# Kernel tuning notes

Measured on AMD Instinct MI355X. Metric: run time of the kernel, lower is better.

## Reference

```python
import jax, jax.numpy as jnp
import numpy as np

SIGMA = 1.0
EPSILON = 1.0
MAX_ITER = 10


def pairwise_kernel(x, y, sigma=SIGMA):
    # k = -||x-y||^2 / (2 sigma^2), shape [B, L, K]
    outer = jnp.einsum('bld,bkd->blk', x, y)
    nx = jnp.sum(x * x, axis=2)
    ny = jnp.sum(y * y, axis=2)
    dist = jnp.clip(nx[:, :, None] + ny[:, None, :] - 2.0 * outer, 0.0, None)
    return -dist / (2.0 * sigma ** 2)


def c_transform(potential, log_weight, kernel, epsilon=EPSILON):
    # rho=None => scale=1, lse = -eps * logsumexp(kernel/eps + (pot/eps + log_w))
    s = potential / epsilon + log_weight            # [B, K]
    operand = kernel / epsilon + s[:, None, :]      # [B, L, K]
    return -epsilon * jax.scipy.special.logsumexp(operand, axis=2)


def potentials(kxy, log_a, log_b):
    kyx = jnp.swapaxes(kxy, 1, 2)
    f0 = jnp.zeros_like(log_a)
    g0 = jnp.zeros_like(log_b)

    def step(carry, _):
        f, g = carry
        fn = c_transform(g, log_b, kxy)
        gn = c_transform(f, log_a, kyx)
        return ((fn + f) * 0.5, (gn + g) * 0.5), None

    (f, g), _ = jax.lax.scan(step, (f0, g0), None, length=MAX_ITER)
    return f, g


def sym_potential(x, log_a):
    kxx = pairwise_kernel(x, x)
    f0 = jnp.zeros_like(log_a)

    def step(f, _):
        fn = c_transform(f, log_a, kxx)
        return (fn + f) * 0.5, None

    f, _ = jax.lax.scan(step, f0, None, length=MAX_ITER)
    return f


def evaluate_potential(x, a, y, b, g):
    # phi_transform is identity for rho=None; scaled_dot_prod forward = sum(a*f, dim=1)
    kxy = pairwise_kernel(x, y)
    f = c_transform(g, jnp.log(b), kxy)
    return jnp.sum(a * f, axis=1)


def setup_inputs() -> dict:
    key = jax.random.key(0)
    k1, k2, k3, k4 = jax.random.split(key, 4)
    B, L, K, D = 8, 2048, 2048, 32
    x = jax.random.normal(k1, (B, L, D), dtype=jnp.float32)
    y = jax.random.normal(k2, (B, K, D), dtype=jnp.float32)
    a = jax.random.uniform(k3, (B, L), dtype=jnp.float32, minval=0.1, maxval=1.0)
    b = jax.random.uniform(k4, (B, K), dtype=jnp.float32, minval=0.1, maxval=1.0)
    a = a / jnp.sum(a, axis=1, keepdims=True)
    b = b / jnp.sum(b, axis=1, keepdims=True)
    return {"x": x, "a": a, "y": y, "b": b}


def reference(x, a, y, b):
    log_a, log_b = jnp.log(a), jnp.log(b)
    kxy = pairwise_kernel(x, y)
    f, g = potentials(kxy, log_a, log_b)
    dist = evaluate_potential(x, a, y, b, g) + evaluate_potential(y, b, x, a, f)
    fx = sym_potential(x, log_a)
    fy = sym_potential(y, log_b)
    ent_x = evaluate_potential(x, a, x, a, fx)
    ent_y = evaluate_potential(y, b, y, b, fy)
    return jnp.mean(dist - ent_x - ent_y)
```

## Files before the change

### kernel.cpp

```cpp
#include <hip/hip_runtime.h>
#include <math.h>

#define BATCH 8
#define NPT   2048
#define DIM   32
#define RPB   64
#define STRIPS (RPB / 16)
#define NBLKR (NPT / RPB)
#define CPW   (NPT / 4)
#define NT    (CPW / 16)
#define L2E   1.44269504088896f
#define BN    (BATCH * NPT)

typedef __attribute__((ext_vector_type(8))) _Float16 half8;
typedef __attribute__((ext_vector_type(4))) float floatx4;
typedef unsigned short u16;
typedef unsigned int u32;

__device__ __forceinline__ u16 f2h_bits(float v) {
    _Float16 h = (_Float16)v;
    return *(u16*)&h;
}
__device__ __forceinline__ float exp2v(float x) { return __builtin_amdgcn_exp2f(x); }

struct CtSet {
    const u16* Ah;
    const u16* Bh;
    const float* tls;
    const float* qX;
    const float* bmIn;
    const float* cwNext;
    const float* prev;
    float* out;
    float* tlsOut;
    float* bmOut;
};
struct CtArgs { CtSet s[4]; int average; };

__global__ __launch_bounds__(256, 4) void ct_kernel(CtArgs args) {
    const int bid  = blockIdx.x;
    const int batch = bid & 7;
    const int rest  = bid >> 3;
    const int slice = rest & 3;
    const int xb    = rest >> 2;
    const CtSet cs = args.s[slice];
    const int row0 = xb * RPB;
    const int tid  = threadIdx.x;
    const int w = tid >> 6, lane = tid & 63, n = lane & 15, quad = lane >> 4;
    const int qk = quad * 8;
    const size_t pbase = (size_t)batch * NPT * DIM;
    const size_t vbase = (size_t)batch * NPT;

    __shared__ float lsum[RPB][4];

    const u16* __restrict__ Ah = cs.Ah + pbase;
    const u16* __restrict__ Bh = cs.Bh + pbase;
    const float* __restrict__ tls = cs.tls + vbase;

    half8 ah[STRIPS];
    #pragma unroll
    for (int s = 0; s < STRIPS; s++) {
        size_t off = (size_t)(row0 + s * 16 + n) * DIM + qk;
        ah[s] = *(const half8*)(Ah + off);
    }

    float tmv = fmaxf(cs.bmIn[batch * 128 + lane], cs.bmIn[batch * 128 + 64 + lane]);
    #pragma unroll
    for (int m = 1; m < 64; m <<= 1) tmv = fmaxf(tmv, __shfl_xor(tmv, m, 64));
    const float Tmax = tmv;
    const float l2eTmax = L2E * Tmax;

    float sum[STRIPS][4];
    #pragma unroll
    for (int s = 0; s < STRIPS; s++)
        #pragma unroll
        for (int r = 0; r < 4; r++) sum[s][r] = 0.0f;

    const int c0 = w * CPW + n;
    const u16* bp = Bh + (size_t)c0 * DIM + qk;
    const float* tp = tls + c0;

    half8 bb[4];
    float tt[4];
    bb[0] = *(const half8*)bp;                       tt[0] = tp[0];
    bb[1] = *(const half8*)(bp + (size_t)16 * DIM);  tt[1] = tp[16];

    auto tile = [&](half8 b, float t) {
        float bias = t - l2eTmax;
        floatx4 ci = (floatx4){bias, bias, bias, bias};
        floatx4 acc[STRIPS];
        #pragma unroll
        for (int s = 0; s < STRIPS; s++)
            acc[s] = __builtin_amdgcn_mfma_f32_16x16x32_f16(ah[s], b, ci, 0, 0, 0);
        #pragma unroll
        for (int s = 0; s < STRIPS; s++)
            #pragma unroll
            for (int r = 0; r < 4; r++)
                sum[s][r] += exp2v(acc[s][r]);
    };

    #pragma unroll 1
    for (int ch = 0; ch < NT; ch += 4) {
        #pragma unroll
        for (int j = 0; j < 4; j++) {
            int nx = ch + j + 2;
            int nxc = nx < NT ? nx : NT - 1;
            bb[(j + 2) & 3] = *(const half8*)(bp + (size_t)nxc * 16 * DIM);
            tt[(j + 2) & 3] = tp[nxc * 16];
            tile(bb[j], tt[j]);
        }
    }

    #pragma unroll
    for (int s = 0; s < STRIPS; s++)
        #pragma unroll
        for (int r = 0; r < 4; r++) {
            float v = sum[s][r];
            #pragma unroll
            for (int m = 1; m < 16; m <<= 1) v += __shfl_xor(v, m, 64);
            if (n == 0) lsum[s * 16 + quad * 4 + r][w] = v;
        }
    __syncthreads();

    if (tid < RPB) {
        float T = (lsum[tid][0] + lsum[tid][1]) + (lsum[tid][2] + lsum[tid][3]);
        int l = row0 + tid;
        float lse = Tmax + __logf(T);
        float val = cs.qX[vbase + l] - lse;
        if (args.average) val = 0.5f * (cs.prev[vbase + l] + val);
        cs.out[vbase + l] = val;
        float tc = val + cs.cwNext[vbase + l];
        cs.tlsOut[vbase + l] = L2E * tc;
        float bm = tc;
        #pragma unroll
        for (int m = 1; m < 16; m <<= 1) bm = fmaxf(bm, __shfl_xor(bm, m, 64));
        if ((tid & 15) == 0)
            cs.bmOut[batch * 128 + xb * STRIPS + (tid >> 4)] = bm;
    }
}

struct InitArgs {
    const float *x, *a, *y, *b;
    float *c_x, *c_y, *qx, *qy;
    u16 *xh, *yh, *xsh, *ysh;
    float *f0, *g0, *fx0, *fy0;
    float *tlsF0, *tlsG0, *tlsFx0, *tlsFy0;
    float *bmF0, *bmG0, *bmFx0, *bmFy0;
};

__global__ __launch_bounds__(256) void init_kernel(InitArgs ia) {
    int idx = blockIdx.x * 256 + threadIdx.x;
    if (idx >= BN) return;
    const float* xp = ia.x + (size_t)idx * DIM;
    const float* yp = ia.y + (size_t)idx * DIM;
    u32* xhp  = (u32*)ia.xh  + (size_t)idx * (DIM / 2);
    u32* yhp  = (u32*)ia.yh  + (size_t)idx * (DIM / 2);
    u32* xshp = (u32*)ia.xsh + (size_t)idx * (DIM / 2);
    u32* yshp = (u32*)ia.ysh + (size_t)idx * (DIM / 2);
    float sx = 0.f, sy = 0.f;
    #pragma unroll
    for (int d = 0; d < DIM; d += 2) {
        float v0 = xp[d], v1 = xp[d + 1];
        sx += v0 * v0 + v1 * v1;
        xhp[d / 2]  = (u32)f2h_bits(v0) | ((u32)f2h_bits(v1) << 16);
        xshp[d / 2] = (u32)f2h_bits(L2E * v0) | ((u32)f2h_bits(L2E * v1) << 16);
        float u0 = yp[d], u1 = yp[d + 1];
        sy += u0 * u0 + u1 * u1;
        yhp[d / 2]  = (u32)f2h_bits(u0) | ((u32)f2h_bits(u1) << 16);
        yshp[d / 2] = (u32)f2h_bits(L2E * u0) | ((u32)f2h_bits(L2E * u1) << 16);
    }
    float qxv = 0.5f * sx, qyv = 0.5f * sy;
    ia.qx[idx] = qxv; ia.qy[idx] = qyv;
    float cxv = __logf(ia.a[idx]) - qxv;
    float cyv = __logf(ia.b[idx]) - qyv;
    ia.c_x[idx] = cxv; ia.c_y[idx] = cyv;
    ia.f0[idx] = 0.f; ia.g0[idx] = 0.f; ia.fx0[idx] = 0.f; ia.fy0[idx] = 0.f;
    ia.tlsF0[idx] = L2E * cxv; ia.tlsG0[idx] = L2E * cyv;
    ia.tlsFx0[idx] = L2E * cxv; ia.tlsFy0[idx] = L2E * cyv;
    float mx = cxv, my = cyv;
    #pragma unroll
    for (int m = 1; m < 16; m <<= 1) {
        mx = fmaxf(mx, __shfl_xor(mx, m, 32));
        my = fmaxf(my, __shfl_xor(my, m, 32));
    }
    if ((threadIdx.x & 15) == 0) {
        int g = idx >> 4;
        ia.bmF0[g] = mx; ia.bmFx0[g] = mx;
        ia.bmG0[g] = my; ia.bmFy0[g] = my;
    }
}

__global__ __launch_bounds__(1024) void reduce_kernel(
        const float* __restrict__ a, const float* __restrict__ b,
        const float* __restrict__ ctA, const float* __restrict__ ctB,
        const float* __restrict__ ctX, const float* __restrict__ ctY,
        float* __restrict__ out) {
    float acc = 0.f;
    for (int idx = threadIdx.x; idx < BN; idx += 1024) {
        acc += a[idx] * (ctA[idx] - ctX[idx]) + b[idx] * (ctB[idx] - ctY[idx]);
    }
    #pragma unroll
    for (int off = 32; off > 0; off >>= 1) acc += __shfl_down(acc, off, 64);
    __shared__ float sm[16];
    if ((threadIdx.x & 63) == 0) sm[threadIdx.x >> 6] = acc;
    __syncthreads();
    if (threadIdx.x == 0) {
        float t = 0.f;
        #pragma unroll
        for (int i = 0; i < 16; i++) t += sm[i];
        out[0] = t / (float)BATCH;
    }
}

extern "C" void kernel_launch(void* const* d_in, const int* in_sizes, int n_in,
                              void* d_out, int out_size, void* d_ws, size_t ws_size,
                              hipStream_t stream) {
    const float* x = (const float*)d_in[0];
    const float* a = (const float*)d_in[1];
    const float* y = (const float*)d_in[2];
    const float* b = (const float*)d_in[3];
    float* out = (float*)d_out;

    float* ws = (float*)d_ws;
    float* c_x = ws + 0 * BN;
    float* c_y = ws + 1 * BN;
    float* qx  = ws + 2 * BN;
    float* qy  = ws + 3 * BN;
    float* fb[2]  = { ws + 4 * BN,  ws + 5 * BN };
    float* gb[2]  = { ws + 6 * BN,  ws + 7 * BN };
    float* fxb[2] = { ws + 8 * BN,  ws + 9 * BN };
    float* fyb[2] = { ws + 10 * BN, ws + 11 * BN };
    float* ctA = ws + 12 * BN;
    float* ctB = ws + 13 * BN;
    float* ctX = ws + 14 * BN;
    float* ctY = ws + 15 * BN;
    float* tlsF[2]  = { ws + 16 * BN, ws + 17 * BN };
    float* tlsG[2]  = { ws + 18 * BN, ws + 19 * BN };
    float* tlsFx[2] = { ws + 20 * BN, ws + 21 * BN };
    float* tlsFy[2] = { ws + 22 * BN, ws + 23 * BN };
    float* dummyT = ws + 24 * BN;
    float* small = ws + 25 * BN;
    float* bmF[2]  = { small + 0 * 1024, small + 1 * 1024 };
    float* bmG[2]  = { small + 2 * 1024, small + 3 * 1024 };
    float* bmFx[2] = { small + 4 * 1024, small + 5 * 1024 };
    float* bmFy[2] = { small + 6 * 1024, small + 7 * 1024 };
    float* dummyB = small + 8 * 1024;
    u16* bf = (u16*)(small + 10 * 1024);
    const size_t AS = (size_t)BN * DIM;
    u16* xh  = bf + 0 * AS;
    u16* yh  = bf + 1 * AS;
    u16* xsh = bf + 2 * AS;
    u16* ysh = bf + 3 * AS;

    InitArgs ia;
    ia.x = x; ia.a = a; ia.y = y; ia.b = b;
    ia.c_x = c_x; ia.c_y = c_y; ia.qx = qx; ia.qy = qy;
    ia.xh = xh; ia.yh = yh; ia.xsh = xsh; ia.ysh = ysh;
    ia.f0 = fb[0]; ia.g0 = gb[0]; ia.fx0 = fxb[0]; ia.fy0 = fyb[0];
    ia.tlsF0 = tlsF[0]; ia.tlsG0 = tlsG[0]; ia.tlsFx0 = tlsFx[0]; ia.tlsFy0 = tlsFy[0];
    ia.bmF0 = bmF[0]; ia.bmG0 = bmG[0]; ia.bmFx0 = bmFx[0]; ia.bmFy0 = bmFy[0];
    init_kernel<<<BN / 256, 256, 0, stream>>>(ia);

    const int nblk = NBLKR * 4 * BATCH;
    int cur = 0;
    for (int it = 0; it < 10; it++) {
        CtArgs ar;
        ar.average = 1;
        ar.s[0] = { xh, ysh, tlsG[cur], qx, bmG[cur], c_x,
                    fb[cur], fb[1 - cur], tlsF[1 - cur], bmF[1 - cur] };
        ar.s[1] = { yh, xsh, tlsF[cur], qy, bmF[cur], c_y,
                    gb[cur], gb[1 - cur], tlsG[1 - cur], bmG[1 - cur] };
        ar.s[2] = { xh, xsh, tlsFx[cur], qx, bmFx[cur], c_x,
                    fxb[cur], fxb[1 - cur], tlsFx[1 - cur], bmFx[1 - cur] };
        ar.s[3] = { yh, ysh, tlsFy[cur], qy, bmFy[cur], c_y,
                    fyb[cur], fyb[1 - cur], tlsFy[1 - cur], bmFy[1 - cur] };
        ct_kernel<<<nblk, 256, 0, stream>>>(ar);
        cur ^= 1;
    }

    CtArgs fin;
    fin.average = 0;
    fin.s[0] = { xh, ysh, tlsG[cur], qx, bmG[cur], c_x, fb[cur], ctA, dummyT, dummyB };
    fin.s[1] = { yh, xsh, tlsF[cur], qy, bmF[cur], c_y, gb[cur], ctB, dummyT, dummyB };
    fin.s[2] = { xh, xsh, tlsFx[cur], qx, bmFx[cur], c_x, fxb[cur], ctX, dummyT, dummyB };
    fin.s[3] = { yh, ysh, tlsFy[cur], qy, bmFy[cur], c_y, fyb[cur], ctY, dummyT, dummyB };
    ct_kernel<<<nblk, 256, 0, stream>>>(fin);

    reduce_kernel<<<1, 1024, 0, stream>>>(a, b, ctA, ctB, ctX, ctY, out);
}
```

Baseline: 283.1 us.

## Switch cost tiles to 32x32 MFMA and fold column bias as multiplicative weight

The log-sum-exp kernel moves from four 16x16x32 f16 MFMAs per column tile, with the bias preloaded into the accumulator, to pairs of 32x32x16 MFMAs that cover 32 rows by 32 columns each. The per-column bias is no longer added before the exponent: it becomes a weight exp2(t - Tmax) applied with an FMA after exponentiating the raw product. The goal is to cut per-column operand loads and MFMA instruction overhead and to get more reuse from each B fragment. In exchange it uses more registers (occupancy hint drops from 4 to 3) and the separate exponentials could lose range or precision compared with a single fused exponent.

```diff
diff --git a/kernel.cpp b/kernel.cpp
--- a/kernel.cpp
+++ b/kernel.cpp
@@ -5,15 +5,14 @@
 #define NPT   2048
 #define DIM   32
 #define RPB   64
-#define STRIPS (RPB / 16)
 #define NBLKR (NPT / RPB)
 #define CPW   (NPT / 4)
-#define NT    (CPW / 16)
+#define NT32  (CPW / 32)
 #define L2E   1.44269504088896f
 #define BN    (BATCH * NPT)
 
 typedef __attribute__((ext_vector_type(8))) _Float16 half8;
-typedef __attribute__((ext_vector_type(4))) float floatx4;
+typedef __attribute__((ext_vector_type(16))) float floatx16;
 typedef unsigned short u16;
 typedef unsigned int u32;
 
@@ -37,7 +36,7 @@
 };
 struct CtArgs { CtSet s[4]; int average; };
 
-__global__ __launch_bounds__(256, 4) void ct_kernel(CtArgs args) {
+__global__ __launch_bounds__(256, 3) void ct_kernel(CtArgs args) {
     const int bid  = blockIdx.x;
     const int batch = bid & 7;
     const int rest  = bid >> 3;
@@ -46,8 +45,9 @@
     const CtSet cs = args.s[slice];
     const int row0 = xb * RPB;
     const int tid  = threadIdx.x;
-    const int w = tid >> 6, lane = tid & 63, n = lane & 15, quad = lane >> 4;
-    const int qk = quad * 8;
+    const int w = tid >> 6, lane = tid & 63;
+    const int l31 = lane & 31, kh = lane >> 5;
+    const int kq = kh * 8;
     const size_t pbase = (size_t)batch * NPT * DIM;
     const size_t vbase = (size_t)batch * NPT;
 
@@ -57,11 +57,12 @@
     const u16* __restrict__ Bh = cs.Bh + pbase;
     const float* __restrict__ tls = cs.tls + vbase;
 
-    half8 ah[STRIPS];
-    #pragma unroll
-    for (int s = 0; s < STRIPS; s++) {
-        size_t off = (size_t)(row0 + s * 16 + n) * DIM + qk;
-        ah[s] = *(const half8*)(Ah + off);
+    half8 ahg[2][2];
+    #pragma unroll
+    for (int g = 0; g < 2; g++) {
+        size_t off = (size_t)(row0 + g * 32 + l31) * DIM + kq;
+        ahg[g][0] = *(const half8*)(Ah + off);
+        ahg[g][1] = *(const half8*)(Ah + off + 16);
     }
 
     float tmv = fmaxf(cs.bmIn[batch * 128 + lane], cs.bmIn[batch * 128 + 64 + lane]);
@@ -70,55 +71,59 @@
     const float Tmax = tmv;
     const float l2eTmax = L2E * Tmax;
 
-    float sum[STRIPS][4];
-    #pragma unroll
-    for (int s = 0; s < STRIPS; s++)
-        #pragma unroll
-        for (int r = 0; r < 4; r++) sum[s][r] = 0.0f;
-
-    const int c0 = w * CPW + n;
-    const u16* bp = Bh + (size_t)c0 * DIM + qk;
-    const float* tp = tls + c0;
-
-    half8 bb[4];
-    float tt[4];
-    bb[0] = *(const half8*)bp;                       tt[0] = tp[0];
-    bb[1] = *(const half8*)(bp + (size_t)16 * DIM);  tt[1] = tp[16];
-
-    auto tile = [&](half8 b, float t) {
-        float bias = t - l2eTmax;
-        floatx4 ci = (floatx4){bias, bias, bias, bias};
-        floatx4 acc[STRIPS];
-        #pragma unroll
-        for (int s = 0; s < STRIPS; s++)
-            acc[s] = __builtin_amdgcn_mfma_f32_16x16x32_f16(ah[s], b, ci, 0, 0, 0);
-        #pragma unroll
-        for (int s = 0; s < STRIPS; s++)
+    float sum[2][16];
+    #pragma unroll
+    for (int g = 0; g < 2; g++)
+        #pragma unroll
+        for (int r = 0; r < 16; r++) sum[g][r] = 0.0f;
+
+    floatx16 z;
+    #pragma unroll
+    for (int r = 0; r < 16; r++) z[r] = 0.0f;
+
+    const u16* bp = Bh + (size_t)(w * CPW + l31) * DIM + kq;
+    const float* tp = tls + w * CPW + l31;
+
+    half8 ba[2], bb2[2];
+    float tt[2];
+    ba[0]  = *(const half8*)bp;
+    bb2[0] = *(const half8*)(bp + 16);
+    tt[0]  = tp[0];
+
+    auto tile = [&](int slot) {
+        float wq = exp2v(tt[slot] - l2eTmax);
+        #pragma unroll
+        for (int g = 0; g < 2; g++) {
+            floatx16 acc = __builtin_amdgcn_mfma_f32_32x32x16_f16(ahg[g][0], ba[slot], z, 0, 0, 0);
+            acc = __builtin_amdgcn_mfma_f32_32x32x16_f16(ahg[g][1], bb2[slot], acc, 0, 0, 0);
             #pragma unroll
-            for (int r = 0; r < 4; r++)
-                sum[s][r] += exp2v(acc[s][r]);
+            for (int r = 0; r < 16; r++)
+                sum[g][r] = fmaf(wq, exp2v(acc[r]), sum[g][r]);
+        }
     };
 
     #pragma unroll 1
-    for (int ch = 0; ch < NT; ch += 4) {
-        #pragma unroll
-        for (int j = 0; j < 4; j++) {
-            int nx = ch + j + 2;
-            int nxc = nx < NT ? nx : NT - 1;
-            bb[(j + 2) & 3] = *(const half8*)(bp + (size_t)nxc * 16 * DIM);
-            tt[(j + 2) & 3] = tp[nxc * 16];
-            tile(bb[j], tt[j]);
-        }
-    }
-
-    #pragma unroll
-    for (int s = 0; s < STRIPS; s++)
-        #pragma unroll
-        for (int r = 0; r < 4; r++) {
-            float v = sum[s][r];
+    for (int ch = 0; ch < NT32; ch += 2) {
+        ba[1]  = *(const half8*)(bp + (size_t)(ch + 1) * 32 * DIM);
+        bb2[1] = *(const half8*)(bp + (size_t)(ch + 1) * 32 * DIM + 16);
+        tt[1]  = tp[(ch + 1) * 32];
+        tile(0);
+        int nx = (ch + 2 < NT32) ? ch + 2 : NT32 - 1;
+        ba[0]  = *(const half8*)(bp + (size_t)nx * 32 * DIM);
+        bb2[0] = *(const half8*)(bp + (size_t)nx * 32 * DIM + 16);
+        tt[0]  = tp[nx * 32];
+        tile(1);
+    }
+
+    #pragma unroll
+    for (int g = 0; g < 2; g++)
+        #pragma unroll
+        for (int r = 0; r < 16; r++) {
+            float v = sum[g][r];
             #pragma unroll
-            for (int m = 1; m < 16; m <<= 1) v += __shfl_xor(v, m, 64);
-            if (n == 0) lsum[s * 16 + quad * 4 + r][w] = v;
+            for (int m = 1; m < 32; m <<= 1) v += __shfl_xor(v, m, 64);
+            if (l31 == 0)
+                lsum[g * 32 + (r & 3) + 8 * (r >> 2) + 4 * kh][w] = v;
         }
     __syncthreads();
 
@@ -135,7 +140,7 @@
         #pragma unroll
         for (int m = 1; m < 16; m <<= 1) bm = fmaxf(bm, __shfl_xor(bm, m, 64));
         if ((tid & 15) == 0)
-            cs.bmOut[batch * 128 + xb * STRIPS + (tid >> 4)] = bm;
+            cs.bmOut[batch * 128 + xb * (RPB / 16) + (tid >> 4)] = bm;
     }
 }
 
```

Result: slower. 338.9 us (+19.7%).
